# Kernel tuning notes

Measured on AMD Instinct MI355X. Metric: run time of the kernel, lower is better.

Reference implementation:

```python
import jax, jax.numpy as jnp
import numpy as np

OUTPUT_DIM = 2000
INPUT_DIM = 8192
N_COLS = 2000  # must equal OUTPUT_DIM so bias broadcasts over last dim as in the torch code
SPARSITY = 0.9
BLOCK = 4


def _apply_block_sparsity(weight, block=BLOCK, sparsity=SPARSITY, seed=1234):
    # Zero out 4x4 blocks with probability `sparsity`, mirroring apply_block_sparsity.
    rng = np.random.RandomState(seed)
    rb = (weight.shape[0] + block - 1) // block
    cb = (weight.shape[1] + block - 1) // block
    keep = (rng.rand(rb, cb) <= (1.0 - sparsity)).astype(np.float32)
    mask = np.kron(keep, np.ones((block, block), dtype=np.float32))
    return weight * mask[: weight.shape[0], : weight.shape[1]]


def setup_inputs() -> dict:
    key = jax.random.key(0)
    k_w, k_b, k_x = jax.random.split(key, 3)
    weight = np.asarray(jax.random.normal(k_w, (OUTPUT_DIM, INPUT_DIM), dtype=jnp.float32))
    weight = jnp.asarray(_apply_block_sparsity(weight))
    bias = jax.random.normal(k_b, (OUTPUT_DIM,), dtype=jnp.float32)
    x = jax.random.normal(k_x, (INPUT_DIM, N_COLS), dtype=jnp.float32)
    return {"weight": weight, "bias": bias, "x": x}


def reference(weight, bias, x):
    # [OUT, IN] @ [IN, N] -> [OUT, N]; bias [OUT] broadcasts over last dim (N == OUT here),
    # exactly matching torch.matmul(weight, x) + bias.
    return jnp.matmul(weight, x) + bias
```

## Files before the change

### kernel.cpp

```cpp
#include <hip/hip_runtime.h>

#define K_DIM 8192
#define M_REAL 2000
#define N_REAL 2000
#define M_PAD 2048
#define N_PAD 2048

#define BM 128
#define BN 128
#define BK 32
#define SPLITK 4
#define KSLAB (K_DIM / SPLITK)

#define NB_CONVW 8192
#define NB_CONVX 4096
#define NB_INIT  3907

typedef __bf16 bf16x8 __attribute__((ext_vector_type(8)));
typedef float f32x4 __attribute__((ext_vector_type(4)));

__device__ __forceinline__ unsigned short f2bf(float f) {
    union { float f; unsigned u; } v; v.f = f;
    unsigned r = v.u + 0x7FFFu + ((v.u >> 16) & 1u);
    return (unsigned short)(r >> 16);
}

__device__ __forceinline__ void async16(const void* g, void* l) {
    __builtin_amdgcn_global_load_lds((__attribute__((address_space(1))) void*)(g),
                                     (__attribute__((address_space(3))) void*)(l),
                                     16, 0, 0);
}

__global__ __launch_bounds__(256) void prep_kernel(const float* __restrict__ W,
                                                   const float* __restrict__ X,
                                                   const float* __restrict__ bias,
                                                   unsigned short* __restrict__ Wb,
                                                   unsigned short* __restrict__ XT,
                                                   float* __restrict__ out) {
    __shared__ unsigned short tile[64][65];
    int bid = blockIdx.x;
    if (bid < NB_CONVW) {
        long long t = (long long)bid * 256 + threadIdx.x;
        long long e = t * 8;
        int m = (int)(e >> 13);
        ushort4 o0 = make_ushort4(0, 0, 0, 0), o1 = o0;
        if (m < M_REAL) {
            const float4* src = (const float4*)(W + e);
            float4 f0 = src[0], f1 = src[1];
            o0.x = f2bf(f0.x); o0.y = f2bf(f0.y); o0.z = f2bf(f0.z); o0.w = f2bf(f0.w);
            o1.x = f2bf(f1.x); o1.y = f2bf(f1.y); o1.z = f2bf(f1.z); o1.w = f2bf(f1.w);
        }
        *(ushort4*)(Wb + e) = o0;
        *(ushort4*)(Wb + e + 4) = o1;
    } else if (bid < NB_CONVW + NB_CONVX) {
        int b2 = bid - NB_CONVW;
        int k0 = (b2 & 127) * 64;
        int n0 = (b2 >> 7) * 64;
        int tx = threadIdx.x & 63;
        int ty = threadIdx.x >> 6;
        int n = n0 + tx;
#pragma unroll
        for (int it = 0; it < 16; ++it) {
            int k = k0 + ty + it * 4;
            float v = (n < N_REAL) ? X[(long long)k * N_REAL + n] : 0.0f;
            tile[ty + it * 4][tx] = f2bf(v);
        }
        __syncthreads();
        int kx = (threadIdx.x & 31) * 2;
        int ny = threadIdx.x >> 5;
#pragma unroll
        for (int it = 0; it < 8; ++it) {
            int nn = ny + it * 8;
            unsigned a = tile[kx][nn];
            unsigned b = tile[kx + 1][nn];
            *(unsigned*)(&XT[(long long)(n0 + nn) * K_DIM + k0 + kx]) = a | (b << 16);
        }
    } else {
        int t = (bid - NB_CONVW - NB_CONVX) * 256 + threadIdx.x;
        if (t < M_REAL * (N_REAL / 4)) {
            int m = t / (N_REAL / 4);
            int n4 = t - m * (N_REAL / 4);
            float4 bv = *(const float4*)(bias + n4 * 4);
            *(float4*)(out + (long long)m * N_REAL + n4 * 4) = bv;
        }
    }
}

__global__ __launch_bounds__(256) void gemm_kernel(const unsigned short* __restrict__ Wb,
                                                   const unsigned short* __restrict__ XT,
                                                   float* __restrict__ out) {
    __shared__ __align__(16) unsigned short As[BM * BK];
    __shared__ __align__(16) unsigned short Bs[BN * BK];

    int f = blockIdx.x;
    int xcd = f & 7;
    int local = f >> 3;
    int lz = local & 3;
    int lx = (local >> 2) & 3;
    int ly = local >> 4;
    int bx = (xcd & 3) * 4 + lx;
    int by = (xcd >> 2) * 8 + ly;
    int bz = lz;

    int t = threadIdx.x;
    int w = t >> 6;
    int l = t & 63;
    int wm = (w >> 1) * 64;
    int wn = (w & 1) * 64;
    int lane16 = l & 15;
    int quad = l >> 4;
    int m0 = by * BM;
    int n0 = bx * BN;
    int ks = bz * KSLAB;

    f32x4 acc[4][4] = {};

    int srow = l >> 2;
    int scol = (l & 3) * 8;
    int rb = w * 32;
    const unsigned short* gA0 = Wb + (long long)(m0 + rb + srow) * K_DIM + ks + scol;
    const unsigned short* gA1 = gA0 + 16LL * K_DIM;
    const unsigned short* gB0 = XT + (long long)(n0 + rb + srow) * K_DIM + ks + scol;
    const unsigned short* gB1 = gB0 + 16LL * K_DIM;
    unsigned short* lA0 = &As[rb * BK];
    unsigned short* lA1 = &As[(rb + 16) * BK];
    unsigned short* lB0 = &Bs[rb * BK];
    unsigned short* lB1 = &Bs[(rb + 16) * BK];

    for (int kt = 0; kt < KSLAB / BK; ++kt) {
        async16(gA0, lA0);
        async16(gA1, lA1);
        async16(gB0, lB0);
        async16(gB1, lB1);
        gA0 += BK; gA1 += BK; gB0 += BK; gB1 += BK;
        __builtin_amdgcn_s_waitcnt(0);
        __syncthreads();

        bf16x8 a[4], b[4];
#pragma unroll
        for (int i = 0; i < 4; ++i)
            a[i] = *(const bf16x8*)&As[(wm + i * 16 + lane16) * BK + quad * 8];
#pragma unroll
        for (int j = 0; j < 4; ++j)
            b[j] = *(const bf16x8*)&Bs[(wn + j * 16 + lane16) * BK + quad * 8];

#pragma unroll
        for (int i = 0; i < 4; ++i)
#pragma unroll
            for (int j = 0; j < 4; ++j)
                acc[i][j] = __builtin_amdgcn_mfma_f32_16x16x32_bf16(a[i], b[j], acc[i][j], 0, 0, 0);

        __syncthreads();
    }

#pragma unroll
    for (int j = 0; j < 4; ++j) {
        int n = n0 + wn + j * 16 + lane16;
        if (n >= N_REAL) continue;
#pragma unroll
        for (int i = 0; i < 4; ++i) {
            int mbase = m0 + wm + i * 16 + quad * 4;
#pragma unroll
            for (int r = 0; r < 4; ++r) {
                int m = mbase + r;
                if (m < M_REAL)
                    atomicAdd(&out[(long long)m * N_REAL + n], acc[i][j][r]);
            }
        }
    }
}

extern "C" void kernel_launch(void* const* d_in, const int* in_sizes, int n_in,
                              void* d_out, int out_size, void* d_ws, size_t ws_size,
                              hipStream_t stream) {
    const float* W    = (const float*)d_in[0];
    const float* bias = (const float*)d_in[1];
    const float* X    = (const float*)d_in[2];
    float* out = (float*)d_out;

    unsigned short* Wb = (unsigned short*)d_ws;
    unsigned short* XT = Wb + (long long)M_PAD * K_DIM;

    prep_kernel<<<NB_CONVW + NB_CONVX + NB_INIT, 256, 0, stream>>>(W, X, bias, Wb, XT, out);

    gemm_kernel<<<(N_PAD / BN) * (M_PAD / BM) * SPLITK, 256, 0, stream>>>(Wb, XT, out);
}
```

Measured before the change: 283.8 us.

## Double-buffer GEMM with 256x256 tiles and split prep into vectorized kernels

The GEMM block tile grows from 128x128 to 256x256 with 512 threads. Shared-memory tiles are now double-buffered, so the next K-slice is loaded asynchronously while the current one is computed, using raw barriers and partial vmcnt waits in place of full waits. The fused prep kernel becomes three launches (W conversion, a float4-vectorized X transpose, bias init). This cuts sync stalls and global traffic per FLOP, at the cost of only 256 workgroups (about one per CU), higher register pressure, and extra kernel launches.

New measurement: 275.9 us. 2.8% less time.

```diff
diff --git a/kernel.cpp b/kernel.cpp
--- a/kernel.cpp
+++ b/kernel.cpp
@@ -6,18 +6,22 @@
 #define M_PAD 2048
 #define N_PAD 2048
 
-#define BM 128
-#define BN 128
+#define BM 256
+#define BN 256
 #define BK 32
 #define SPLITK 4
 #define KSLAB (K_DIM / SPLITK)
+#define NIT (KSLAB / BK)
 
 #define NB_CONVW 8192
-#define NB_CONVX 4096
 #define NB_INIT  3907
 
 typedef __bf16 bf16x8 __attribute__((ext_vector_type(8)));
 typedef float f32x4 __attribute__((ext_vector_type(4)));
+
+#define RAW_BARRIER()  asm volatile("s_barrier" ::: "memory")
+#define WAIT_VM4()     asm volatile("s_waitcnt vmcnt(4)" ::: "memory")
+#define WAIT_VM0()     asm volatile("s_waitcnt vmcnt(0)" ::: "memory")
 
 __device__ __forceinline__ unsigned short f2bf(float f) {
     union { float f; unsigned u; } v; v.f = f;
@@ -31,89 +35,89 @@
                                      16, 0, 0);
 }
 
-__global__ __launch_bounds__(256) void prep_kernel(const float* __restrict__ W,
-                                                   const float* __restrict__ X,
-                                                   const float* __restrict__ bias,
-                                                   unsigned short* __restrict__ Wb,
-                                                   unsigned short* __restrict__ XT,
+__global__ __launch_bounds__(256) void conv_w_kernel(const float* __restrict__ W,
+                                                     unsigned short* __restrict__ Wb) {
+    long long t = (long long)blockIdx.x * 256 + threadIdx.x;
+    long long e = t * 8;
+    int m = (int)(e >> 13);
+    ushort4 o0 = make_ushort4(0, 0, 0, 0), o1 = o0;
+    if (m < M_REAL) {
+        const float4* src = (const float4*)(W + e);
+        float4 f0 = src[0], f1 = src[1];
+        o0.x = f2bf(f0.x); o0.y = f2bf(f0.y); o0.z = f2bf(f0.z); o0.w = f2bf(f0.w);
+        o1.x = f2bf(f1.x); o1.y = f2bf(f1.y); o1.z = f2bf(f1.z); o1.w = f2bf(f1.w);
+    }
+    *(ushort4*)(Wb + e) = o0;
+    *(ushort4*)(Wb + e + 4) = o1;
+}
+
+__global__ __launch_bounds__(256) void conv_xt_kernel(const float* __restrict__ X,
+                                                      unsigned short* __restrict__ XT) {
+    __shared__ unsigned short tile[64][68];
+    int k0 = blockIdx.x * 64;
+    int n0 = blockIdx.y * 64;
+    int t = threadIdx.x;
+    int c16 = t & 15, r16 = t >> 4;
+#pragma unroll
+    for (int it = 0; it < 4; ++it) {
+        int k = k0 + r16 + it * 16;
+        int n = n0 + c16 * 4;
+        float4 v = make_float4(0.f, 0.f, 0.f, 0.f);
+        if (n < N_REAL) v = *(const float4*)(X + (long long)k * N_REAL + n);
+        ushort4 o;
+        o.x = f2bf(v.x); o.y = f2bf(v.y); o.z = f2bf(v.z); o.w = f2bf(v.w);
+        *(ushort4*)&tile[r16 + it * 16][c16 * 4] = o;
+    }
+    __syncthreads();
+#pragma unroll
+    for (int it = 0; it < 4; ++it) {
+        int nn = r16 + it * 16;
+        int k4 = c16 * 4;
+        ushort4 o;
+        o.x = tile[k4 + 0][nn];
+        o.y = tile[k4 + 1][nn];
+        o.z = tile[k4 + 2][nn];
+        o.w = tile[k4 + 3][nn];
+        *(ushort4*)(XT + (long long)(n0 + nn) * K_DIM + k0 + k4) = o;
+    }
+}
+
+__global__ __launch_bounds__(256) void bias_kernel(const float* __restrict__ bias,
                                                    float* __restrict__ out) {
-    __shared__ unsigned short tile[64][65];
-    int bid = blockIdx.x;
-    if (bid < NB_CONVW) {
-        long long t = (long long)bid * 256 + threadIdx.x;
-        long long e = t * 8;
-        int m = (int)(e >> 13);
-        ushort4 o0 = make_ushort4(0, 0, 0, 0), o1 = o0;
-        if (m < M_REAL) {
-            const float4* src = (const float4*)(W + e);
-            float4 f0 = src[0], f1 = src[1];
-            o0.x = f2bf(f0.x); o0.y = f2bf(f0.y); o0.z = f2bf(f0.z); o0.w = f2bf(f0.w);
-            o1.x = f2bf(f1.x); o1.y = f2bf(f1.y); o1.z = f2bf(f1.z); o1.w = f2bf(f1.w);
-        }
-        *(ushort4*)(Wb + e) = o0;
-        *(ushort4*)(Wb + e + 4) = o1;
-    } else if (bid < NB_CONVW + NB_CONVX) {
-        int b2 = bid - NB_CONVW;
-        int k0 = (b2 & 127) * 64;
-        int n0 = (b2 >> 7) * 64;
-        int tx = threadIdx.x & 63;
-        int ty = threadIdx.x >> 6;
-        int n = n0 + tx;
-#pragma unroll
-        for (int it = 0; it < 16; ++it) {
-            int k = k0 + ty + it * 4;
-            float v = (n < N_REAL) ? X[(long long)k * N_REAL + n] : 0.0f;
-            tile[ty + it * 4][tx] = f2bf(v);
-        }
-        __syncthreads();
-        int kx = (threadIdx.x & 31) * 2;
-        int ny = threadIdx.x >> 5;
-#pragma unroll
-        for (int it = 0; it < 8; ++it) {
-            int nn = ny + it * 8;
-            unsigned a = tile[kx][nn];
-            unsigned b = tile[kx + 1][nn];
-            *(unsigned*)(&XT[(long long)(n0 + nn) * K_DIM + k0 + kx]) = a | (b << 16);
-        }
-    } else {
-        int t = (bid - NB_CONVW - NB_CONVX) * 256 + threadIdx.x;
-        if (t < M_REAL * (N_REAL / 4)) {
-            int m = t / (N_REAL / 4);
-            int n4 = t - m * (N_REAL / 4);
-            float4 bv = *(const float4*)(bias + n4 * 4);
-            *(float4*)(out + (long long)m * N_REAL + n4 * 4) = bv;
-        }
-    }
-}
-
-__global__ __launch_bounds__(256) void gemm_kernel(const unsigned short* __restrict__ Wb,
-                                                   const unsigned short* __restrict__ XT,
-                                                   float* __restrict__ out) {
-    __shared__ __align__(16) unsigned short As[BM * BK];
-    __shared__ __align__(16) unsigned short Bs[BN * BK];
+    int t = blockIdx.x * 256 + threadIdx.x;
+    if (t < M_REAL * (N_REAL / 4)) {
+        int m = t / (N_REAL / 4);
+        int n4 = t - m * (N_REAL / 4);
+        float4 bv = *(const float4*)(bias + n4 * 4);
+        *(float4*)(out + (long long)m * N_REAL + n4 * 4) = bv;
+    }
+}
+
+__global__ __launch_bounds__(512, 2) void gemm_kernel(const unsigned short* __restrict__ Wb,
+                                                      const unsigned short* __restrict__ XT,
+                                                      float* __restrict__ out) {
+    __shared__ __align__(16) unsigned short As[2][BM * BK];
+    __shared__ __align__(16) unsigned short Bs[2][BN * BK];
 
     int f = blockIdx.x;
     int xcd = f & 7;
     int local = f >> 3;
-    int lz = local & 3;
-    int lx = (local >> 2) & 3;
-    int ly = local >> 4;
-    int bx = (xcd & 3) * 4 + lx;
-    int by = (xcd >> 2) * 8 + ly;
-    int bz = lz;
+    int bz = local & 3;
+    int bx = (xcd & 3) * 2 + ((local >> 2) & 1);
+    int by = (xcd >> 2) * 4 + (local >> 3);
 
     int t = threadIdx.x;
     int w = t >> 6;
     int l = t & 63;
-    int wm = (w >> 1) * 64;
-    int wn = (w & 1) * 64;
+    int wm = (w >> 2) * 128;
+    int wn = (w & 3) * 64;
     int lane16 = l & 15;
     int quad = l >> 4;
     int m0 = by * BM;
     int n0 = bx * BN;
     int ks = bz * KSLAB;
 
-    f32x4 acc[4][4] = {};
+    f32x4 acc[8][4] = {};
 
     int srow = l >> 2;
     int scol = (l & 3) * 8;
@@ -122,35 +126,44 @@
     const unsigned short* gA1 = gA0 + 16LL * K_DIM;
     const unsigned short* gB0 = XT + (long long)(n0 + rb + srow) * K_DIM + ks + scol;
     const unsigned short* gB1 = gB0 + 16LL * K_DIM;
-    unsigned short* lA0 = &As[rb * BK];
-    unsigned short* lA1 = &As[(rb + 16) * BK];
-    unsigned short* lB0 = &Bs[rb * BK];
-    unsigned short* lB1 = &Bs[(rb + 16) * BK];
-
-    for (int kt = 0; kt < KSLAB / BK; ++kt) {
-        async16(gA0, lA0);
-        async16(gA1, lA1);
-        async16(gB0, lB0);
-        async16(gB1, lB1);
-        gA0 += BK; gA1 += BK; gB0 += BK; gB1 += BK;
-        __builtin_amdgcn_s_waitcnt(0);
-        __syncthreads();
-
-        bf16x8 a[4], b[4];
-#pragma unroll
-        for (int i = 0; i < 4; ++i)
-            a[i] = *(const bf16x8*)&As[(wm + i * 16 + lane16) * BK + quad * 8];
+
+    async16(gA0, &As[0][rb * BK]);
+    async16(gA1, &As[0][(rb + 16) * BK]);
+    async16(gB0, &Bs[0][rb * BK]);
+    async16(gB1, &Bs[0][(rb + 16) * BK]);
+    gA0 += BK; gA1 += BK; gB0 += BK; gB1 += BK;
+
+    for (int kt = 0; kt < NIT; ++kt) {
+        int cur = kt & 1;
+        if (kt + 1 < NIT) {
+            int nxt = cur ^ 1;
+            async16(gA0, &As[nxt][rb * BK]);
+            async16(gA1, &As[nxt][(rb + 16) * BK]);
+            async16(gB0, &Bs[nxt][rb * BK]);
+            async16(gB1, &Bs[nxt][(rb + 16) * BK]);
+            gA0 += BK; gA1 += BK; gB0 += BK; gB1 += BK;
+            WAIT_VM4();
+        } else {
+            WAIT_VM0();
+        }
+        RAW_BARRIER();
+
+        bf16x8 a[8], b[4];
+#pragma unroll
+        for (int i = 0; i < 8; ++i)
+            a[i] = *(const bf16x8*)&As[cur][(wm + i * 16 + lane16) * BK + quad * 8];
 #pragma unroll
         for (int j = 0; j < 4; ++j)
-            b[j] = *(const bf16x8*)&Bs[(wn + j * 16 + lane16) * BK + quad * 8];
-
-#pragma unroll
-        for (int i = 0; i < 4; ++i)
+            b[j] = *(const bf16x8*)&Bs[cur][(wn + j * 16 + lane16) * BK + quad * 8];
+
+#pragma unroll
+        for (int i = 0; i < 8; ++i)
 #pragma unroll
             for (int j = 0; j < 4; ++j)
                 acc[i][j] = __builtin_amdgcn_mfma_f32_16x16x32_bf16(a[i], b[j], acc[i][j], 0, 0, 0);
 
-        __syncthreads();
+        if (kt + 1 < NIT)
+            RAW_BARRIER();
     }
 
 #pragma unroll
@@ -158,7 +171,7 @@
         int n = n0 + wn + j * 16 + lane16;
         if (n >= N_REAL) continue;
 #pragma unroll
-        for (int i = 0; i < 4; ++i) {
+        for (int i = 0; i < 8; ++i) {
             int mbase = m0 + wm + i * 16 + quad * 4;
 #pragma unroll
             for (int r = 0; r < 4; ++r) {
@@ -181,7 +194,10 @@
     unsigned short* Wb = (unsigned short*)d_ws;
     unsigned short* XT = Wb + (long long)M_PAD * K_DIM;
 
-    prep_kernel<<<NB_CONVW + NB_CONVX + NB_INIT, 256, 0, stream>>>(W, X, bias, Wb, XT, out);
-
-    gemm_kernel<<<(N_PAD / BN) * (M_PAD / BM) * SPLITK, 256, 0, stream>>>(Wb, XT, out);
-}
+    conv_w_kernel<<<NB_CONVW, 256, 0, stream>>>(W, Wb);
+    dim3 tgrid(K_DIM / 64, N_PAD / 64);
+    conv_xt_kernel<<<tgrid, 256, 0, stream>>>(X, XT);
+    bias_kernel<<<NB_INIT, 256, 0, stream>>>(bias, out);
+
+    gemm_kernel<<<(N_PAD / BN) * (M_PAD / BM) * SPLITK, 512, 0, stream>>>(Wb, XT, out);
+}
```
